# Performance work log

Hardware: AMD Instinct MI355X
Metric: run time of the kernel (lower is better)

Reference implementation:

```python
import jax, jax.numpy as jnp
import numpy as np

LN_EPS = 1e-5


def _forward(x, conv_w, conv_b, ln_w, ln_b, in_proj_w, in_proj_b, out_proj_w, out_proj_b):
    # x: (1, duration, dimensions)
    B, Dur, Dim = x.shape
    xt = jnp.transpose(x, (0, 2, 1))  # (1, Dim, Dur) -> Conv1d NCH layout
    branches = []
    for b in range(Dur):  # structural loop over the 32 conv branches (kernel size k=b+1)
        k = b + 1
        L = Dur - b  # output length duration - k + 1
        w = conv_w[b, :, :, :k]  # (Dim_out, Dim_in, k); padded taps beyond k unused
        y = jax.lax.conv_general_dilated(
            xt, w, window_strides=(1,), padding='VALID',
            dimension_numbers=('NCH', 'OIH', 'NCH'))  # (1, Dim, L)
        y = y + conv_b[b][None, :, None]
        y = jax.nn.gelu(y, approximate=False)  # torch nn.GELU default is exact erf form
        # LayerNorm(normalized_shape=[1, Dim, L]) with batch==1 normalizes the whole tensor
        mu = jnp.mean(y)
        var = jnp.var(y)  # biased, matching torch LayerNorm
        y = (y - mu) * jax.lax.rsqrt(var + LN_EPS)
        y = y * ln_w[b, :, :L][None] + ln_b[b, :, :L][None]
        branches.append(y)  # dropout is identity at inference (p=0.0)
    xc = jnp.concatenate(branches, axis=2)  # (1, Dim, T), T = Dur*(Dur+1)//2
    T = xc.shape[2]

    # nn.MultiheadAttention(embed_dim=T, num_heads=T), batch_first=False: input (L=1, N=Dim, E=T).
    # With seq_len==1, softmax over the single key is exactly 1, so attention output is
    # out_proj(v_proj(value)). value_i = x[:, i, :] broadcast over N, so every batch row of
    # output_i equals out_proj(v_proj(xc[0, i])). Summing over i (the feature loop):
    Wv = in_proj_w[2 * T:]          # (T, T) value slice of in_proj
    bv = in_proj_b[2 * T:]          # (T,)
    V = xc[0] @ Wv.T + bv           # (Dim, T): row i is v-proj of feature i
    S = V.sum(axis=0) @ out_proj_w.T + Dim * out_proj_b  # (T,)  sum over the Dim-term loop
    xa = jnp.broadcast_to(S[None, None, :], (1, Dim, T))  # identical rows, as in torch

    # x.unfold(2, Dur, 4*Dur).mean(-1)
    step = 4 * Dur
    n_w = (T - Dur) // step + 1
    idx = jnp.arange(n_w)[:, None] * step + jnp.arange(Dur)[None, :]  # (n_w, Dur)
    pooled = xa[:, :, idx].mean(-1)  # (1, Dim, n_w)
    return jnp.transpose(pooled, (0, 2, 1))  # (1, n_w, Dim)


def setup_inputs() -> dict:
    key = jax.random.key(0)
    ks = jax.random.split(key, 6)
    Dur, Dim = 32, 256
    T = Dur * (Dur + 1) // 2  # 528
    x = jax.random.normal(ks[0], (1, Dur, Dim), jnp.float32)
    conv_w = jax.random.normal(ks[1], (Dur, Dim, Dim, Dur), jnp.float32) * 0.02  # padded kernel bank
    conv_b = jax.random.normal(ks[2], (Dur, Dim), jnp.float32) * 0.02
    ln_w = jnp.ones((Dur, Dim, Dur), jnp.float32)   # branch b uses [:, :, :Dur-b]
    ln_b = jnp.zeros((Dur, Dim, Dur), jnp.float32)
    in_proj_w = jax.random.normal(ks[3], (3 * T, T), jnp.float32) * 0.02
    in_proj_b = jnp.zeros((3 * T,), jnp.float32)
    out_proj_w = jax.random.normal(ks[4], (T, T), jnp.float32) * 0.02
    out_proj_b = jnp.zeros((T,), jnp.float32)
    return {"x": x, "conv_w": conv_w, "conv_b": conv_b, "ln_w": ln_w, "ln_b": ln_b,
            "in_proj_w": in_proj_w, "in_proj_b": in_proj_b,
            "out_proj_w": out_proj_w, "out_proj_b": out_proj_b}


def reference(x, conv_w, conv_b, ln_w, ln_b, in_proj_w, in_proj_b, out_proj_w, out_proj_b):
    return _forward(x, conv_w, conv_b, ln_w, ln_b, in_proj_w, in_proj_b, out_proj_w, out_proj_b)
```

## Files before the change

kernel.cpp:

```cpp
#include <hip/hip_runtime.h>
#include <math.h>

#define DUR 32
#define DIM 256
#define TT  528

#define WS_BSUM 0
#define WS_BSQ  32
#define WS_CY   64
#define WS_CW   592
#define WS_CB   1120
#define WS_S    1648
#define WS_ZERO_FLOATS 592

__device__ __forceinline__ float gelu_exact(float v) {
    return 0.5f * v * (1.0f + erff(v * 0.70710678118654752f));
}

__device__ __forceinline__ float wave_reduce_down(float v) {
    v += __shfl_down(v, 32, 64);
    v += __shfl_down(v, 16, 64);
    v += __shfl_down(v, 8, 64);
    v += __shfl_down(v, 4, 64);
    v += __shfl_down(v, 2, 64);
    v += __shfl_down(v, 1, 64);
    return v;
}

template<int K4>
__device__ __forceinline__ void wave_body(
    const int bb, const int o, const int lane,
    const float* __restrict__ x, const float* __restrict__ W,
    const float* __restrict__ convb, const float* __restrict__ lnw,
    float* __restrict__ ws)
{
    const int k = bb + 1;
    const int L = DUR - bb;
    constexpr int MAXL = (36 - 4 * K4) > 32 ? 32 : (36 - 4 * K4);

    const float* Wo = W + (size_t)(bb * DIM + o) * (DIM * DUR);

    float4 wb[2][K4];
    {
        const float* Wl = Wo + (size_t)lane * DUR;
#pragma unroll
        for (int m = 0; m < K4; ++m) wb[0][m] = *(const float4*)(Wl + 4 * m);
    }

    float acc[MAXL];
#pragma unroll
    for (int t = 0; t < MAXL; ++t) acc[t] = 0.f;

#pragma unroll 1
    for (int c = 0; c < 4; ++c) {
        const int cur = c & 1;
        if (c < 3) {
            const float* Wl = Wo + (size_t)((c + 1) * 64 + lane) * DUR;
#pragma unroll
            for (int m = 0; m < K4; ++m) wb[cur ^ 1][m] = *(const float4*)(Wl + 4 * m);
        }
        const int i = c * 64 + lane;
        float xv[35];
#pragma unroll
        for (int tau = 0; tau < 32; ++tau) xv[tau] = x[tau * DIM + i];
        xv[32] = 0.f; xv[33] = 0.f; xv[34] = 0.f;
#pragma unroll
        for (int m = 0; m < K4; ++m) {
            if (4 * m + 1 >= k) wb[cur][m].y = 0.f;
            if (4 * m + 2 >= k) wb[cur][m].z = 0.f;
            if (4 * m + 3 >= k) wb[cur][m].w = 0.f;
        }
#pragma unroll
        for (int t = 0; t < MAXL; ++t) {
            if (t < L) {
#pragma unroll
                for (int m = 0; m < K4; ++m) {
                    acc[t] = fmaf(xv[t + 4*m + 0], wb[cur][m].x, acc[t]);
                    acc[t] = fmaf(xv[t + 4*m + 1], wb[cur][m].y, acc[t]);
                    acc[t] = fmaf(xv[t + 4*m + 2], wb[cur][m].z, acc[t]);
                    acc[t] = fmaf(xv[t + 4*m + 3], wb[cur][m].w, acc[t]);
                }
            }
        }
    }

    float mine = 0.f;
#pragma unroll
    for (int t = 0; t < MAXL; ++t) {
        if (t < L) {
            float v = acc[t];
            v += __shfl_xor(v, 1, 64);
            v += __shfl_xor(v, 2, 64);
            v += __shfl_xor(v, 4, 64);
            v += __shfl_xor(v, 8, 64);
            v += __shfl_xor(v, 16, 64);
            v += __shfl_xor(v, 32, 64);
            if (lane == t) mine = v;
        }
    }

    const int tg = bb * DUR - (bb * (bb - 1)) / 2;
    float g = 0.f;
    if (lane < L) {
        const float y = mine + convb[bb * DIM + o];
        g = gelu_exact(y);
        const float lw = lnw[((size_t)(bb * DIM + o)) * DUR + lane];
        atomicAdd(ws + WS_CY + tg + lane, g * lw);
    }
    const float s1 = wave_reduce_down(g);
    const float s2 = wave_reduce_down(g * g);
    if (lane == 0) {
        atomicAdd(ws + WS_BSUM + bb, s1);
        atomicAdd(ws + WS_BSQ  + bb, s2);
    }
}

__global__ __launch_bounds__(256, 4) void conv_kernel(
    const float* __restrict__ x, const float* __restrict__ W,
    const float* __restrict__ convb, const float* __restrict__ lnw,
    const float* __restrict__ lnb, float* __restrict__ ws)
{
    const int bid = blockIdx.x;
    const int n = threadIdx.x;
    if (bid >= 2048) {
        const int pb = bid - 2048;
        int b = 0, off = 0;
        while (pb >= off + (DUR - b)) { off += DUR - b; ++b; }
        const int t = pb - off;
        const float lw = lnw[((size_t)(b * DIM + n)) * DUR + t];
        const float lb = lnb[((size_t)(b * DIM + n)) * DUR + t];
        __shared__ float rw[4], rb[4];
        const int wave = n >> 6, lane = n & 63;
        const float a = wave_reduce_down(lw);
        const float c = wave_reduce_down(lb);
        if (lane == 0) { rw[wave] = a; rb[wave] = c; }
        __syncthreads();
        if (n == 0) {
            ws[WS_CW + pb] = rw[0] + rw[1] + rw[2] + rw[3];
            ws[WS_CB + pb] = rb[0] + rb[1] + rb[2] + rb[3];
        }
        return;
    }

    const int p    = bid & 15;
    const int og   = bid >> 4;
    const int w    = n >> 6;
    const int lane = n & 63;
    const int bb   = (w < 2) ? p : 31 - p;
    const int o    = og * 2 + (w & 1);
    switch (bb >> 2) {
        case 0:  wave_body<1>(bb, o, lane, x, W, convb, lnw, ws); break;
        case 1:  wave_body<2>(bb, o, lane, x, W, convb, lnw, ws); break;
        case 2:  wave_body<3>(bb, o, lane, x, W, convb, lnw, ws); break;
        case 3:  wave_body<4>(bb, o, lane, x, W, convb, lnw, ws); break;
        case 4:  wave_body<5>(bb, o, lane, x, W, convb, lnw, ws); break;
        case 5:  wave_body<6>(bb, o, lane, x, W, convb, lnw, ws); break;
        case 6:  wave_body<7>(bb, o, lane, x, W, convb, lnw, ws); break;
        default: wave_body<8>(bb, o, lane, x, W, convb, lnw, ws); break;
    }
}

__global__ __launch_bounds__(256) void proj1_kernel(
    float* ws, const float* __restrict__ in_proj_w,
    const float* __restrict__ in_proj_b)
{
    __shared__ float cc[TT];
    __shared__ float mu_s[32], r_s[32];
    __shared__ int map[TT];
    const int n = threadIdx.x;
    if (n < 32) {
        const int Lb = 32 - n;
        const float cnt = 256.f * (float)Lb;
        const float mu = ws[WS_BSUM + n] / cnt;
        const float var = ws[WS_BSQ + n] / cnt - mu * mu;
        mu_s[n] = mu;
        r_s[n] = rsqrtf(var + 1e-5f);
        const int off = n * 32 - (n * (n - 1)) / 2;
        for (int t = 0; t < Lb; ++t) map[off + t] = n;
    }
    __syncthreads();
    for (int t = n; t < TT; t += 256) {
        const int b = map[t];
        cc[t] = (ws[WS_CY + t] - mu_s[b] * ws[WS_CW + t]) * r_s[b] + ws[WS_CB + t];
    }
    __syncthreads();
    const int wave = n >> 6, lane = n & 63;
    const int row = blockIdx.x * 4 + wave;
    const float* Wr = in_proj_w + (size_t)(2 * TT + row) * TT;
    float a = 0.f;
    for (int t = lane; t < TT; t += 64) a = fmaf(Wr[t], cc[t], a);
    a = wave_reduce_down(a);
    if (lane == 0) ws[WS_S + row] = a + 256.f * in_proj_b[2 * TT + row];
}

__global__ __launch_bounds__(256) void proj2_kernel(
    const float* __restrict__ ws, const float* __restrict__ out_proj_w,
    const float* __restrict__ out_proj_b, float* __restrict__ out)
{
    const int w = blockIdx.x, n = threadIdx.x;
    const int wave = n >> 6, lane = n & 63;
    __shared__ float s2s[32];
    __shared__ float mv;
    for (int jj = 0; jj < 8; ++jj) {
        const int j = wave * 8 + jj;
        const int u = w * 128 + j;
        const float* Or = out_proj_w + (size_t)u * TT;
        float a = 0.f;
        for (int t = lane; t < TT; t += 64) a = fmaf(Or[t], ws[WS_S + t], a);
        a = wave_reduce_down(a);
        if (lane == 0) s2s[j] = a + 256.f * out_proj_b[u];
    }
    __syncthreads();
    if (n < 64) {
        float v = (n < 32) ? s2s[n] : 0.f;
        v += __shfl_down(v, 16, 64);
        v += __shfl_down(v, 8, 64);
        v += __shfl_down(v, 4, 64);
        v += __shfl_down(v, 2, 64);
        v += __shfl_down(v, 1, 64);
        if (n == 0) mv = v * (1.0f / 32.0f);
    }
    __syncthreads();
    out[w * 256 + n] = mv;
}

extern "C" void kernel_launch(void* const* d_in, const int* in_sizes, int n_in,
                              void* d_out, int out_size, void* d_ws, size_t ws_size,
                              hipStream_t stream)
{
    const float* x   = (const float*)d_in[0];
    const float* W   = (const float*)d_in[1];
    const float* cb  = (const float*)d_in[2];
    const float* lnw = (const float*)d_in[3];
    const float* lnb = (const float*)d_in[4];
    const float* ipw = (const float*)d_in[5];
    const float* ipb = (const float*)d_in[6];
    const float* opw = (const float*)d_in[7];
    const float* opb = (const float*)d_in[8];
    float* ws  = (float*)d_ws;
    float* out = (float*)d_out;

    hipMemsetAsync(ws, 0, WS_ZERO_FLOATS * sizeof(float), stream);
    conv_kernel<<<2048 + TT, 256, 0, stream>>>(x, W, cb, lnw, lnb, ws);
    proj1_kernel<<<132, 256, 0, stream>>>(ws, ipw, ipb);
    proj2_kernel<<<4, 256, 0, stream>>>(ws, opw, opb, out);
}
```

Measured before the change: 506.9 us.

## Fully unroll conv chunk loop with two-deep weight prefetch and remap blocks

Replaces the runtime chunk loop and indexed double buffer with fully unrolled code that keeps two named weight buffers and issues weight loads two chunks ahead of compute. Empty asm barriers pin x and weight values in VGPRs so the compiler cannot sink or rematerialize them. Launch bounds drop to 3 blocks per CU to allow more registers, and block indices are remapped so consecutive blocks share a branch pair but differ in output channel. This trades occupancy and register pressure for deeper memory overlap.

```diff
diff --git a/kernel.cpp b/kernel.cpp
--- a/kernel.cpp
+++ b/kernel.cpp
@@ -40,49 +40,61 @@
 
     const float* Wo = W + (size_t)(bb * DIM + o) * (DIM * DUR);
 
-    float4 wb[2][K4];
-    {
-        const float* Wl = Wo + (size_t)lane * DUR;
-#pragma unroll
-        for (int m = 0; m < K4; ++m) wb[0][m] = *(const float4*)(Wl + 4 * m);
-    }
-
     float acc[MAXL];
 #pragma unroll
     for (int t = 0; t < MAXL; ++t) acc[t] = 0.f;
 
-#pragma unroll 1
-    for (int c = 0; c < 4; ++c) {
-        const int cur = c & 1;
-        if (c < 3) {
-            const float* Wl = Wo + (size_t)((c + 1) * 64 + lane) * DUR;
-#pragma unroll
-            for (int m = 0; m < K4; ++m) wb[cur ^ 1][m] = *(const float4*)(Wl + 4 * m);
-        }
-        const int i = c * 64 + lane;
-        float xv[35];
-#pragma unroll
-        for (int tau = 0; tau < 32; ++tau) xv[tau] = x[tau * DIM + i];
-        xv[32] = 0.f; xv[33] = 0.f; xv[34] = 0.f;
-#pragma unroll
-        for (int m = 0; m < K4; ++m) {
-            if (4 * m + 1 >= k) wb[cur][m].y = 0.f;
-            if (4 * m + 2 >= k) wb[cur][m].z = 0.f;
-            if (4 * m + 3 >= k) wb[cur][m].w = 0.f;
-        }
-#pragma unroll
-        for (int t = 0; t < MAXL; ++t) {
-            if (t < L) {
-#pragma unroll
-                for (int m = 0; m < K4; ++m) {
-                    acc[t] = fmaf(xv[t + 4*m + 0], wb[cur][m].x, acc[t]);
-                    acc[t] = fmaf(xv[t + 4*m + 1], wb[cur][m].y, acc[t]);
-                    acc[t] = fmaf(xv[t + 4*m + 2], wb[cur][m].z, acc[t]);
-                    acc[t] = fmaf(xv[t + 4*m + 3], wb[cur][m].w, acc[t]);
-                }
-            }
-        }
-    }
+    float4 wa[K4], wb2[K4];
+
+#define LOAD_CHUNK(BUF, C)                                                   \
+    {                                                                        \
+        const float* Wl = Wo + (size_t)((C) * 64 + lane) * DUR;              \
+        _Pragma("unroll")                                                    \
+        for (int m = 0; m < K4; ++m) BUF[m] = *(const float4*)(Wl + 4 * m);  \
+    }
+
+#define COMPUTE_CHUNK(BUF, C)                                                \
+    {                                                                        \
+        const int i = (C) * 64 + lane;                                       \
+        float xv[35];                                                        \
+        _Pragma("unroll")                                                    \
+        for (int tau = 0; tau < 32; ++tau) xv[tau] = x[tau * DIM + i];       \
+        xv[32] = 0.f; xv[33] = 0.f; xv[34] = 0.f;                            \
+        _Pragma("unroll")                                                    \
+        for (int tau = 0; tau < 35; ++tau) asm volatile("" : "+v"(xv[tau])); \
+        _Pragma("unroll")                                                    \
+        for (int m = 0; m < K4; ++m) {                                       \
+            if (4 * m + 1 >= k) BUF[m].y = 0.f;                              \
+            if (4 * m + 2 >= k) BUF[m].z = 0.f;                              \
+            if (4 * m + 3 >= k) BUF[m].w = 0.f;                              \
+            asm volatile("" : "+v"(BUF[m].x), "+v"(BUF[m].y),                \
+                              "+v"(BUF[m].z), "+v"(BUF[m].w));               \
+        }                                                                    \
+        _Pragma("unroll")                                                    \
+        for (int t = 0; t < MAXL; ++t) {                                     \
+            if (t < L) {                                                     \
+                _Pragma("unroll")                                            \
+                for (int m = 0; m < K4; ++m) {                               \
+                    acc[t] = fmaf(xv[t + 4*m + 0], BUF[m].x, acc[t]);        \
+                    acc[t] = fmaf(xv[t + 4*m + 1], BUF[m].y, acc[t]);        \
+                    acc[t] = fmaf(xv[t + 4*m + 2], BUF[m].z, acc[t]);        \
+                    acc[t] = fmaf(xv[t + 4*m + 3], BUF[m].w, acc[t]);        \
+                }                                                            \
+            }                                                                \
+        }                                                                    \
+    }
+
+    LOAD_CHUNK(wa, 0)
+    LOAD_CHUNK(wb2, 1)
+    COMPUTE_CHUNK(wa, 0)
+    LOAD_CHUNK(wa, 2)
+    COMPUTE_CHUNK(wb2, 1)
+    LOAD_CHUNK(wb2, 3)
+    COMPUTE_CHUNK(wa, 2)
+    COMPUTE_CHUNK(wb2, 3)
+
+#undef LOAD_CHUNK
+#undef COMPUTE_CHUNK
 
     float mine = 0.f;
 #pragma unroll
@@ -115,7 +127,7 @@
     }
 }
 
-__global__ __launch_bounds__(256, 4) void conv_kernel(
+__global__ __launch_bounds__(256, 3) void conv_kernel(
     const float* __restrict__ x, const float* __restrict__ W,
     const float* __restrict__ convb, const float* __restrict__ lnw,
     const float* __restrict__ lnb, float* __restrict__ ws)
@@ -142,8 +154,8 @@
         return;
     }
 
-    const int p    = bid & 15;
-    const int og   = bid >> 4;
+    const int p    = (bid >> 3) & 15;
+    const int og   = (bid & 7) | ((bid >> 7) << 3);
     const int w    = n >> 6;
     const int lane = n & 63;
     const int bb   = (w < 2) ? p : 31 - p;
```

Result: faster. 454.6 us (-10.3%).
